# Performance work log

Measured on AMD Instinct MI355X. Metric: run time of the kernel, lower is better.

The kernel has to match this reference:

```python
import jax, jax.numpy as jnp
import numpy as np

B, T, L, H = 512, 512, 64, 512  # batch, time_steps, sequence_len, hidden_dim


def gru_cell(x, h, W_ih, W_hh, b_ih, b_hh):
    # PyTorch GRUCell math. W_ih: [3H, in], W_hh: [3H, H]; gate order (r, z, n).
    gi = x @ W_ih.T + b_ih
    gh = h @ W_hh.T + b_hh
    i_r, i_z, i_n = jnp.split(gi, 3, axis=-1)
    h_r, h_z, h_n = jnp.split(gh, 3, axis=-1)
    r = jax.nn.sigmoid(i_r + h_r)
    z = jax.nn.sigmoid(i_z + h_z)
    n = jnp.tanh(i_n + r * h_n)
    return (1.0 - z) * n + z * h


def setup_inputs() -> dict:
    key = jax.random.key(0)
    ks = jax.random.split(key, 12)
    s = 1.0 / np.sqrt(H)  # PyTorch GRUCell/Linear init scale
    u = lambda k, shape: jax.random.uniform(k, shape, jnp.float32, -s, s)
    return {
        "x": jax.random.normal(ks[0], (B, T + L - 1), jnp.float32),
        "h_1": jnp.zeros((B, H), jnp.float32),
        "h_2": jnp.zeros((B, H), jnp.float32),
        "W_ih1": u(ks[1], (3 * H, T)),
        "W_hh1": u(ks[2], (3 * H, H)),
        "b_ih1": u(ks[3], (3 * H,)),
        "b_hh1": u(ks[4], (3 * H,)),
        "W_ih2": u(ks[5], (3 * H, H)),
        "W_hh2": u(ks[6], (3 * H, H)),
        "b_ih2": u(ks[7], (3 * H,)),
        "b_hh2": u(ks[8], (3 * H,)),
        "W_fc": u(ks[9], (1, H)),
        "b_fc": u(ks[10], (1,)),
    }


def reference(x, h_1, h_2, W_ih1, W_hh1, b_ih1, b_hh1,
              W_ih2, W_hh2, b_ih2, b_hh2, W_fc, b_fc):
    # Sliding windows x[:, t:t+T] for t in [0, L): gather once, scan over steps.
    idx = jnp.arange(L)[:, None] + jnp.arange(T)[None, :]  # [L, T]
    xs = jnp.transpose(x[:, idx], (1, 0, 2))  # [L, B, T]

    def step(carry, x_t):
        h1, h2 = carry
        h1 = gru_cell(x_t, h1, W_ih1, W_hh1, b_ih1, b_hh1)
        h2 = gru_cell(h1, h2, W_ih2, W_hh2, b_ih2, b_hh2)
        y = (h2 @ W_fc.T + b_fc)[:, 0]  # [B]
        return (h1, h2), y

    (h1, h2), ys = jax.lax.scan(step, (h_1, h_2), xs)
    return ys.T, h1, h2  # output_seq [B, L], final hidden states
```

## Files before the change

### kernel.cpp

```cpp
#include <hip/hip_runtime.h>
#include <hip/hip_bf16.h>
#include <math.h>

typedef __attribute__((ext_vector_type(8))) short short8;
typedef __attribute__((ext_vector_type(4))) float f32x4;
typedef unsigned short u16;
typedef unsigned int u32;

__device__ __forceinline__ u16 f2bf(float f) {
  union { float f; u32 u; } x; x.f = f;
  return (u16)((x.u + 0x7fffu + ((x.u >> 16) & 1u)) >> 16);
}
__device__ __forceinline__ float sigm(float v) { return 1.0f / (1.0f + __expf(-v)); }

#define MFMA __builtin_amdgcn_mfma_f32_16x16x32_bf16
#define HS 262144

#define LDG16_BODY(FL)                                        \
    "global_load_dwordx4 %0, %16, off " FL "\n\t"             \
    "global_load_dwordx4 %1, %16, off offset:64 " FL "\n\t"   \
    "global_load_dwordx4 %2, %16, off offset:128 " FL "\n\t"  \
    "global_load_dwordx4 %3, %16, off offset:192 " FL "\n\t"  \
    "global_load_dwordx4 %4, %16, off offset:256 " FL "\n\t"  \
    "global_load_dwordx4 %5, %16, off offset:320 " FL "\n\t"  \
    "global_load_dwordx4 %6, %16, off offset:384 " FL "\n\t"  \
    "global_load_dwordx4 %7, %16, off offset:448 " FL "\n\t"  \
    "global_load_dwordx4 %8, %16, off offset:512 " FL "\n\t"  \
    "global_load_dwordx4 %9, %16, off offset:576 " FL "\n\t"  \
    "global_load_dwordx4 %10, %16, off offset:640 " FL "\n\t" \
    "global_load_dwordx4 %11, %16, off offset:704 " FL "\n\t" \
    "global_load_dwordx4 %12, %16, off offset:768 " FL "\n\t" \
    "global_load_dwordx4 %13, %16, off offset:832 " FL "\n\t" \
    "global_load_dwordx4 %14, %16, off offset:896 " FL "\n\t" \
    "global_load_dwordx4 %15, %16, off offset:960 " FL "\n\t" \
    "s_waitcnt vmcnt(0)"
#define LDG16_OPS(a, base)                                                     \
    : "=&v"(a[0]), "=&v"(a[1]), "=&v"(a[2]), "=&v"(a[3]), "=&v"(a[4]),         \
      "=&v"(a[5]), "=&v"(a[6]), "=&v"(a[7]), "=&v"(a[8]), "=&v"(a[9]),         \
      "=&v"(a[10]), "=&v"(a[11]), "=&v"(a[12]), "=&v"(a[13]), "=&v"(a[14]),    \
      "=&v"(a[15])                                                             \
    : "v"(base) : "memory"

__device__ __forceinline__ void ldg16_sc0(short8 a[16], const u16* base) {
  asm volatile(LDG16_BODY("sc0") LDG16_OPS(a, base));
}
__device__ __forceinline__ void ldg16_sc01(short8 a[16], const u16* base) {
  asm volatile(LDG16_BODY("sc0 sc1") LDG16_OPS(a, base));
}
__device__ __forceinline__ void stg_sc01(u32* p, u32 v) {
  asm volatile("global_store_dword %0, %1, off sc0 sc1" :: "v"(p), "v"(v) : "memory");
}

__device__ __forceinline__ void waits_nf(unsigned* a, unsigned ta, unsigned* b, unsigned tb) {
  if (threadIdx.x == 0) {
    while (__hip_atomic_load(a, __ATOMIC_RELAXED, __HIP_MEMORY_SCOPE_AGENT) < ta)
      __builtin_amdgcn_s_sleep(1);
    while (__hip_atomic_load(b, __ATOMIC_RELAXED, __HIP_MEMORY_SCOPE_AGENT) < tb)
      __builtin_amdgcn_s_sleep(1);
  }
  __syncthreads();
}

__global__ __launch_bounds__(256, 1) void gru_fused(
    const float* __restrict__ xin, const float* __restrict__ h1in, const float* __restrict__ h2in,
    const float* __restrict__ Wih1, const float* __restrict__ Whh1,
    const float* __restrict__ bih1, const float* __restrict__ bhh1,
    const float* __restrict__ Wih2, const float* __restrict__ Whh2,
    const float* __restrict__ bih2, const float* __restrict__ bhh2,
    const float* __restrict__ Wfc, const float* __restrict__ bfc,
    float* __restrict__ out, u16* __restrict__ wsb, unsigned* __restrict__ barc)
{
  const int bid   = blockIdx.x;
  const int rb    = bid & 3;
  const int layer = (bid >> 2) & 1;
  const int cbl   = bid >> 3;
  const int n0    = cbl * 16;
  const int wid   = bid >> 2;
  const int tid   = threadIdx.x;
  const int w     = tid >> 6;
  const int lane  = tid & 63;
  const int quad  = lane >> 4;
  const int m16   = lane & 15;

  u16* x0  = wsb;
  u16* x1  = x0 + 512 * 576;
  u16* h1r = x1 + 512 * 576;
  u16* h2r = h1r + 4 * HS;
  u16* h1m = h2r + 4 * HS;

  __shared__ short8 wlds[96 * 64];

  unsigned* c0    = barc + rb * 32;
  unsigned* c1    = barc + 256 + rb * 32;
  unsigned* cinit = barc + 512;

  const float* Wih = layer ? Wih2 : Wih1;
  const float* Whh = layer ? Whh2 : Whh1;
  const float* bih = layer ? bih2 : bih1;
  const float* bhh = layer ? bhh2 : bhh1;

  for (int i = wid * 256 + tid; i < 128 * 575; i += 64 * 256) {
    int r = i / 575, c = i - r * 575;
    int row = rb * 128 + r;
    u16 bv = f2bf(xin[row * 575 + c]);
    x0[row * 576 + c] = bv;
    if (c >= 1) x1[row * 576 + (c - 1)] = bv;
  }
  for (int i = wid * 256 + tid; i < 128 * 512; i += 64 * 256) {
    int r = i >> 9, c = i & 511;
    int row = rb * 128 + r;
    u16 h1v = f2bf(h1in[row * 512 + c]);
    h1r[3 * HS + row * 512 + c] = h1v;
    h2r[3 * HS + row * 512 + c] = f2bf(h2in[row * 512 + c]);
  }
  for (int i = tid; i < 96 * 64; i += 256) {
    int blk = i >> 6, l = i & 63;
    int s, gr;
    if (blk < 64) { s = blk & 31; gr = (blk >> 5) * 512; }
    else          { s = blk - 64; gr = 1024; }
    int n  = n0 + (l & 15);
    int k0 = s * 32 + (l >> 4) * 8;
    short8 pk;
    #pragma unroll
    for (int j = 0; j < 8; ++j) {
      int k = k0 + j;
      float v = (k < 512) ? Wih[(gr + n) * 512 + k] : Whh[(gr + n) * 512 + (k - 512)];
      pk[j] = (short)f2bf(v);
    }
    wlds[blk * 64 + l] = pk;
  }

  float hreg[2][4];
  const float* hin = layer ? h2in : h1in;
  #pragma unroll
  for (int rf = 0; rf < 2; ++rf)
    #pragma unroll
    for (int q = 0; q < 4; ++q)
      hreg[rf][q] = hin[(rb * 128 + (2 * w + rf) * 16 + quad * 4 + q) * 512 + n0 + m16];

  const int nn = n0 + m16;
  const float bias_r  = bih[nn] + bhh[nn];
  const float bias_z  = bih[512 + nn] + bhh[512 + nn];
  const float bias_in = bih[1024 + nn];
  const float bias_hn = bhh[1024 + nn];
  const float wfc  = Wfc[nn];
  const float bfcv = bfc[0];

  __syncthreads();
  if (tid == 0) {
    __builtin_amdgcn_fence(__ATOMIC_RELEASE, "agent");
    __hip_atomic_fetch_add(cinit, 1u, __ATOMIC_RELAXED, __HIP_MEMORY_SCOPE_AGENT);
    while (__hip_atomic_load(cinit, __ATOMIC_RELAXED, __HIP_MEMORY_SCOPE_AGENT) < 256u)
      __builtin_amdgcn_s_sleep(1);
    __builtin_amdgcn_fence(__ATOMIC_ACQUIRE, "agent");
  }
  __syncthreads();

  const int arow0 = rb * 128 + (2 * w) * 16 + m16;
  const int arow1 = arow0 + 16;

  if (layer == 0) {
    for (int u = 0; u < 64; ++u) {
      f32x4 acc[2][4] = {};
      {
        const int c = u & 1;
        const u16* xc = c ? x1 : x0;
        const u32* pa0 = (const u32*)(xc + (size_t)arow0 * 576 + (u - c) + quad * 8);
        const u32* pa1 = (const u32*)(xc + (size_t)arow1 * 576 + (u - c) + quad * 8);
        #pragma unroll
        for (int s = 0; s < 16; ++s) {
          union { short8 v; u32 u4[4]; } a0, a1;
          #pragma unroll
          for (int j = 0; j < 4; ++j) { a0.u4[j] = pa0[s * 16 + j]; a1.u4[j] = pa1[s * 16 + j]; }
          short8 br = wlds[(s)      * 64 + lane];
          short8 bz = wlds[(32 + s) * 64 + lane];
          short8 bi = wlds[(64 + s) * 64 + lane];
          acc[0][0] = MFMA(a0.v, br, acc[0][0], 0, 0, 0);
          acc[1][0] = MFMA(a1.v, br, acc[1][0], 0, 0, 0);
          acc[0][1] = MFMA(a0.v, bz, acc[0][1], 0, 0, 0);
          acc[1][1] = MFMA(a1.v, bz, acc[1][1], 0, 0, 0);
          acc[0][2] = MFMA(a0.v, bi, acc[0][2], 0, 0, 0);
          acc[1][2] = MFMA(a1.v, bi, acc[1][2], 0, 0, 0);
        }
      }
      waits_nf(c0, 32u * (unsigned)u, c1, u >= 4 ? 32u * (unsigned)(u - 3) : 0u);
      #pragma unroll
      for (int rf = 0; rf < 2; ++rf) {
        short8 a[16];
        const u16* base = h1r + (size_t)((u + 3) & 3) * HS +
                          (size_t)(rf ? arow1 : arow0) * 512 + quad * 8;
        ldg16_sc0(a, base);
        #pragma unroll
        for (int s = 0; s < 16; ++s) {
          short8 br = wlds[(16 + s) * 64 + lane];
          short8 bz = wlds[(48 + s) * 64 + lane];
          short8 bh = wlds[(80 + s) * 64 + lane];
          acc[rf][0] = MFMA(a[s], br, acc[rf][0], 0, 0, 0);
          acc[rf][1] = MFMA(a[s], bz, acc[rf][1], 0, 0, 0);
          acc[rf][3] = MFMA(a[s], bh, acc[rf][3], 0, 0, 0);
        }
      }
      {
        u16* hw = h1r + (size_t)(u & 3) * HS;
        u32* hm = (u32*)(h1m + (size_t)(u & 3) * HS);
        #pragma unroll
        for (int rf = 0; rf < 2; ++rf)
          #pragma unroll
          for (int q = 0; q < 4; ++q) {
            float rg = sigm(acc[rf][0][q] + bias_r);
            float zg = sigm(acc[rf][1][q] + bias_z);
            float ng = tanhf(acc[rf][2][q] + bias_in + rg * (acc[rf][3][q] + bias_hn));
            float hv = (1.0f - zg) * ng + zg * hreg[rf][q];
            hreg[rf][q] = hv;
            int row = rb * 128 + (2 * w + rf) * 16 + quad * 4 + q;
            u16 b = f2bf(hv);
            hw[row * 512 + nn] = b;
            int pb = __shfl_xor((int)(u32)b, 1);
            if (!(m16 & 1))
              stg_sc01(&hm[(row * 512 + nn) >> 1], (u32)b | ((u32)(u16)pb << 16));
          }
      }
      asm volatile("s_waitcnt vmcnt(0)" ::: "memory");
      __syncthreads();
      if (tid == 0)
        __hip_atomic_fetch_add(c0, 1u, __ATOMIC_RELAXED, __HIP_MEMORY_SCOPE_AGENT);
    }
  } else {
    for (int v = 0; v < 64; ++v) {
      f32x4 acc[2][4] = {};
      waits_nf(c1, 32u * (unsigned)v, c0, 32u * (unsigned)(v + 1));
      #pragma unroll
      for (int rf = 0; rf < 2; ++rf) {
        short8 a[16];
        const u16* base = h2r + (size_t)((v + 3) & 3) * HS +
                          (size_t)(rf ? arow1 : arow0) * 512 + quad * 8;
        ldg16_sc0(a, base);
        #pragma unroll
        for (int s = 0; s < 16; ++s) {
          short8 br = wlds[(16 + s) * 64 + lane];
          short8 bz = wlds[(48 + s) * 64 + lane];
          short8 bh = wlds[(80 + s) * 64 + lane];
          acc[rf][0] = MFMA(a[s], br, acc[rf][0], 0, 0, 0);
          acc[rf][1] = MFMA(a[s], bz, acc[rf][1], 0, 0, 0);
          acc[rf][3] = MFMA(a[s], bh, acc[rf][3], 0, 0, 0);
        }
      }
      #pragma unroll
      for (int rf = 0; rf < 2; ++rf) {
        short8 a[16];
        const u16* base = h1m + (size_t)(v & 3) * HS +
                          (size_t)(rf ? arow1 : arow0) * 512 + quad * 8;
        ldg16_sc01(a, base);
        #pragma unroll
        for (int s = 0; s < 16; ++s) {
          short8 br = wlds[(s)      * 64 + lane];
          short8 bz = wlds[(32 + s) * 64 + lane];
          short8 bi = wlds[(64 + s) * 64 + lane];
          acc[rf][0] = MFMA(a[s], br, acc[rf][0], 0, 0, 0);
          acc[rf][1] = MFMA(a[s], bz, acc[rf][1], 0, 0, 0);
          acc[rf][2] = MFMA(a[s], bi, acc[rf][2], 0, 0, 0);
        }
      }
      {
        u16* hw = h2r + (size_t)(v & 3) * HS;
        #pragma unroll
        for (int rf = 0; rf < 2; ++rf)
          #pragma unroll
          for (int q = 0; q < 4; ++q) {
            float rg = sigm(acc[rf][0][q] + bias_r);
            float zg = sigm(acc[rf][1][q] + bias_z);
            float ng = tanhf(acc[rf][2][q] + bias_in + rg * (acc[rf][3][q] + bias_hn));
            float hv = (1.0f - zg) * ng + zg * hreg[rf][q];
            hreg[rf][q] = hv;
            int row = rb * 128 + (2 * w + rf) * 16 + quad * 4 + q;
            hw[row * 512 + nn] = f2bf(hv);
          }
      }
      __syncthreads();
      if (tid == 0)
        __hip_atomic_fetch_add(c1, 1u, __ATOMIC_RELAXED, __HIP_MEMORY_SCOPE_AGENT);
      #pragma unroll
      for (int rf = 0; rf < 2; ++rf)
        #pragma unroll
        for (int q = 0; q < 4; ++q) {
          float yv = hreg[rf][q] * wfc;
          yv += __shfl_xor(yv, 1);
          yv += __shfl_xor(yv, 2);
          yv += __shfl_xor(yv, 4);
          yv += __shfl_xor(yv, 8);
          if (m16 == 0) {
            int row = rb * 128 + (2 * w + rf) * 16 + quad * 4 + q;
            atomicAdd(&out[row * 64 + v], yv + (n0 == 0 ? bfcv : 0.0f));
          }
        }
    }
  }

  float* hout = out + 32768 + layer * (512 * 512);
  #pragma unroll
  for (int rf = 0; rf < 2; ++rf)
    #pragma unroll
    for (int q = 0; q < 4; ++q) {
      int row = rb * 128 + (2 * w + rf) * 16 + quad * 4 + q;
      hout[row * 512 + nn] = hreg[rf][q];
    }
}

extern "C" void kernel_launch(void* const* d_in, const int* in_sizes, int n_in,
                              void* d_out, int out_size, void* d_ws, size_t ws_size,
                              hipStream_t stream) {
  (void)in_sizes; (void)n_in; (void)out_size; (void)ws_size;
  hipMemsetAsync(d_out, 0, 32768 * sizeof(float), stream);
  hipMemsetAsync(d_ws, 0, 4096, stream);
  unsigned* bar = (unsigned*)d_ws;
  u16* wsb = (u16*)((char*)d_ws + 4096);
  gru_fused<<<256, 256, 0, stream>>>(
      (const float*)d_in[0], (const float*)d_in[1], (const float*)d_in[2],
      (const float*)d_in[3], (const float*)d_in[4], (const float*)d_in[5], (const float*)d_in[6],
      (const float*)d_in[7], (const float*)d_in[8], (const float*)d_in[9], (const float*)d_in[10],
      (const float*)d_in[11], (const float*)d_in[12],
      (float*)d_out, wsb, bar);
}
```

Before: 815.7 us.

## Replace atomic counter barriers with per-block flag arrays and split load waits

Replaces the shared atomic-counter barriers with per-column-block flag slots that each block writes with a plain sc0 sc1 store. Waiters poll all 32 flags in parallel with one wave-wide load and a ballot, which removes atomic contention. It also issues both row-fragment loads before waiting and uses a partial vmcnt wait so the first MFMA chain overlaps the second load. Layer 2 now waits on layer 1 only after its own recurrent half, hidden stores are packed into 32-bit writes, and sigmoid/tanh use rcp-based fast approximations. The risks are the memory ordering of plain flag stores without explicit fences, and a small loss of accuracy in the activations.

```diff
diff --git a/kernel.cpp b/kernel.cpp
--- a/kernel.cpp
+++ b/kernel.cpp
@@ -11,7 +11,12 @@
   union { float f; u32 u; } x; x.f = f;
   return (u16)((x.u + 0x7fffu + ((x.u >> 16) & 1u)) >> 16);
 }
-__device__ __forceinline__ float sigm(float v) { return 1.0f / (1.0f + __expf(-v)); }
+__device__ __forceinline__ float sigm(float v) {
+  return __builtin_amdgcn_rcpf(1.0f + __expf(-v));
+}
+__device__ __forceinline__ float tanh_fast(float v) {
+  return 1.0f - 2.0f * __builtin_amdgcn_rcpf(1.0f + __expf(2.0f * v));
+}
 
 #define MFMA __builtin_amdgcn_mfma_f32_16x16x32_bf16
 #define HS 262144
@@ -32,8 +37,7 @@
     "global_load_dwordx4 %12, %16, off offset:768 " FL "\n\t" \
     "global_load_dwordx4 %13, %16, off offset:832 " FL "\n\t" \
     "global_load_dwordx4 %14, %16, off offset:896 " FL "\n\t" \
-    "global_load_dwordx4 %15, %16, off offset:960 " FL "\n\t" \
-    "s_waitcnt vmcnt(0)"
+    "global_load_dwordx4 %15, %16, off offset:960 " FL
 #define LDG16_OPS(a, base)                                                     \
     : "=&v"(a[0]), "=&v"(a[1]), "=&v"(a[2]), "=&v"(a[3]), "=&v"(a[4]),         \
       "=&v"(a[5]), "=&v"(a[6]), "=&v"(a[7]), "=&v"(a[8]), "=&v"(a[9]),         \
@@ -41,24 +45,41 @@
       "=&v"(a[15])                                                             \
     : "v"(base) : "memory"
 
-__device__ __forceinline__ void ldg16_sc0(short8 a[16], const u16* base) {
+__device__ __forceinline__ void ldg16nw_sc0(short8 a[16], const u16* base) {
   asm volatile(LDG16_BODY("sc0") LDG16_OPS(a, base));
 }
-__device__ __forceinline__ void ldg16_sc01(short8 a[16], const u16* base) {
+__device__ __forceinline__ void ldg16nw_sc01(short8 a[16], const u16* base) {
   asm volatile(LDG16_BODY("sc0 sc1") LDG16_OPS(a, base));
 }
+#define VMCNT16() do { asm volatile("s_waitcnt vmcnt(16)" ::: "memory"); \
+                       __builtin_amdgcn_sched_barrier(0); } while (0)
+#define VMCNT0()  do { asm volatile("s_waitcnt vmcnt(0)"  ::: "memory"); \
+                       __builtin_amdgcn_sched_barrier(0); } while (0)
+
 __device__ __forceinline__ void stg_sc01(u32* p, u32 v) {
   asm volatile("global_store_dword %0, %1, off sc0 sc1" :: "v"(p), "v"(v) : "memory");
 }
-
-__device__ __forceinline__ void waits_nf(unsigned* a, unsigned ta, unsigned* b, unsigned tb) {
-  if (threadIdx.x == 0) {
-    while (__hip_atomic_load(a, __ATOMIC_RELAXED, __HIP_MEMORY_SCOPE_AGENT) < ta)
-      __builtin_amdgcn_s_sleep(1);
-    while (__hip_atomic_load(b, __ATOMIC_RELAXED, __HIP_MEMORY_SCOPE_AGENT) < tb)
-      __builtin_amdgcn_s_sleep(1);
-  }
-  __syncthreads();
+__device__ __forceinline__ u32 ldflag(const u32* p) {
+  u32 v;
+  asm volatile("global_load_dword %0, %1, off sc0 sc1\n\t"
+               "s_waitcnt vmcnt(0)" : "=v"(v) : "v"(p) : "memory");
+  return v;
+}
+
+__device__ __forceinline__ u32 wait_ge(const u32* flags, u32 target, int lane) {
+  const u32* p = flags + (lane & 31);
+  u32 v;
+  for (;;) {
+    v = ldflag(p);
+    if (__ballot(v >= target) == ~0ull) break;
+    __builtin_amdgcn_s_sleep(1);
+  }
+  #pragma unroll
+  for (int k = 16; k; k >>= 1) {
+    u32 o = (u32)__shfl_xor((int)v, k);
+    v = v < o ? v : o;
+  }
+  return v;
 }
 
 __global__ __launch_bounds__(256, 1) void gru_fused(
@@ -90,8 +111,8 @@
 
   __shared__ short8 wlds[96 * 64];
 
-  unsigned* c0    = barc + rb * 32;
-  unsigned* c1    = barc + 256 + rb * 32;
+  u32* f0    = (u32*)barc + rb * 32;
+  u32* f1    = (u32*)barc + 128 + rb * 32;
   unsigned* cinit = barc + 512;
 
   const float* Wih = layer ? Wih2 : Wih1;
@@ -160,7 +181,9 @@
   const int arow1 = arow0 + 16;
 
   if (layer == 0) {
+    u32 c1min = 0;
     for (int u = 0; u < 64; ++u) {
+      if (u >= 4 && c1min < (u32)(u - 3)) c1min = wait_ge(f1, (u32)(u - 3), lane);
       f32x4 acc[2][4] = {};
       {
         const int c = u & 1;
@@ -183,102 +206,138 @@
           acc[1][2] = MFMA(a1.v, bi, acc[1][2], 0, 0, 0);
         }
       }
-      waits_nf(c0, 32u * (unsigned)u, c1, u >= 4 ? 32u * (unsigned)(u - 3) : 0u);
-      #pragma unroll
-      for (int rf = 0; rf < 2; ++rf) {
-        short8 a[16];
-        const u16* base = h1r + (size_t)((u + 3) & 3) * HS +
-                          (size_t)(rf ? arow1 : arow0) * 512 + quad * 8;
-        ldg16_sc0(a, base);
+      if (u > 0) wait_ge(f0, (u32)u, lane); else VMCNT0();
+      {
+        short8 a0[16], a1[16];
+        const u16* hb = h1r + (size_t)((u + 3) & 3) * HS + quad * 8;
+        ldg16nw_sc0(a0, hb + (size_t)arow0 * 512);
+        ldg16nw_sc0(a1, hb + (size_t)arow1 * 512);
+        VMCNT16();
         #pragma unroll
         for (int s = 0; s < 16; ++s) {
           short8 br = wlds[(16 + s) * 64 + lane];
           short8 bz = wlds[(48 + s) * 64 + lane];
           short8 bh = wlds[(80 + s) * 64 + lane];
-          acc[rf][0] = MFMA(a[s], br, acc[rf][0], 0, 0, 0);
-          acc[rf][1] = MFMA(a[s], bz, acc[rf][1], 0, 0, 0);
-          acc[rf][3] = MFMA(a[s], bh, acc[rf][3], 0, 0, 0);
-        }
-      }
-      {
-        u16* hw = h1r + (size_t)(u & 3) * HS;
-        u32* hm = (u32*)(h1m + (size_t)(u & 3) * HS);
+          acc[0][0] = MFMA(a0[s], br, acc[0][0], 0, 0, 0);
+          acc[0][1] = MFMA(a0[s], bz, acc[0][1], 0, 0, 0);
+          acc[0][3] = MFMA(a0[s], bh, acc[0][3], 0, 0, 0);
+        }
+        VMCNT0();
+        #pragma unroll
+        for (int s = 0; s < 16; ++s) {
+          short8 br = wlds[(16 + s) * 64 + lane];
+          short8 bz = wlds[(48 + s) * 64 + lane];
+          short8 bh = wlds[(80 + s) * 64 + lane];
+          acc[1][0] = MFMA(a1[s], br, acc[1][0], 0, 0, 0);
+          acc[1][1] = MFMA(a1[s], bz, acc[1][1], 0, 0, 0);
+          acc[1][3] = MFMA(a1[s], bh, acc[1][3], 0, 0, 0);
+        }
+      }
+      {
+        u32* hw32 = (u32*)(h1r + (size_t)(u & 3) * HS);
+        u32* hm   = (u32*)(h1m + (size_t)(u & 3) * HS);
         #pragma unroll
         for (int rf = 0; rf < 2; ++rf)
           #pragma unroll
           for (int q = 0; q < 4; ++q) {
             float rg = sigm(acc[rf][0][q] + bias_r);
             float zg = sigm(acc[rf][1][q] + bias_z);
-            float ng = tanhf(acc[rf][2][q] + bias_in + rg * (acc[rf][3][q] + bias_hn));
+            float ng = tanh_fast(acc[rf][2][q] + bias_in + rg * (acc[rf][3][q] + bias_hn));
             float hv = (1.0f - zg) * ng + zg * hreg[rf][q];
             hreg[rf][q] = hv;
             int row = rb * 128 + (2 * w + rf) * 16 + quad * 4 + q;
             u16 b = f2bf(hv);
-            hw[row * 512 + nn] = b;
             int pb = __shfl_xor((int)(u32)b, 1);
-            if (!(m16 & 1))
-              stg_sc01(&hm[(row * 512 + nn) >> 1], (u32)b | ((u32)(u16)pb << 16));
+            if (!(m16 & 1)) {
+              u32 pr = (u32)b | ((u32)(u16)pb << 16);
+              int pi = (row * 512 + nn) >> 1;
+              hw32[pi] = pr;
+              stg_sc01(&hm[pi], pr);
+            }
           }
       }
       asm volatile("s_waitcnt vmcnt(0)" ::: "memory");
       __syncthreads();
-      if (tid == 0)
-        __hip_atomic_fetch_add(c0, 1u, __ATOMIC_RELAXED, __HIP_MEMORY_SCOPE_AGENT);
+      if (tid == 0) stg_sc01(&f0[cbl], (u32)(u + 1));
     }
   } else {
     for (int v = 0; v < 64; ++v) {
       f32x4 acc[2][4] = {};
-      waits_nf(c1, 32u * (unsigned)v, c0, 32u * (unsigned)(v + 1));
-      #pragma unroll
-      for (int rf = 0; rf < 2; ++rf) {
-        short8 a[16];
-        const u16* base = h2r + (size_t)((v + 3) & 3) * HS +
-                          (size_t)(rf ? arow1 : arow0) * 512 + quad * 8;
-        ldg16_sc0(a, base);
+      if (v > 0) wait_ge(f1, (u32)v, lane); else VMCNT0();
+      {
+        short8 a0[16], a1[16];
+        const u16* hb = h2r + (size_t)((v + 3) & 3) * HS + quad * 8;
+        ldg16nw_sc0(a0, hb + (size_t)arow0 * 512);
+        ldg16nw_sc0(a1, hb + (size_t)arow1 * 512);
+        VMCNT16();
         #pragma unroll
         for (int s = 0; s < 16; ++s) {
           short8 br = wlds[(16 + s) * 64 + lane];
           short8 bz = wlds[(48 + s) * 64 + lane];
           short8 bh = wlds[(80 + s) * 64 + lane];
-          acc[rf][0] = MFMA(a[s], br, acc[rf][0], 0, 0, 0);
-          acc[rf][1] = MFMA(a[s], bz, acc[rf][1], 0, 0, 0);
-          acc[rf][3] = MFMA(a[s], bh, acc[rf][3], 0, 0, 0);
-        }
-      }
-      #pragma unroll
-      for (int rf = 0; rf < 2; ++rf) {
-        short8 a[16];
-        const u16* base = h1m + (size_t)(v & 3) * HS +
-                          (size_t)(rf ? arow1 : arow0) * 512 + quad * 8;
-        ldg16_sc01(a, base);
+          acc[0][0] = MFMA(a0[s], br, acc[0][0], 0, 0, 0);
+          acc[0][1] = MFMA(a0[s], bz, acc[0][1], 0, 0, 0);
+          acc[0][3] = MFMA(a0[s], bh, acc[0][3], 0, 0, 0);
+        }
+        VMCNT0();
+        #pragma unroll
+        for (int s = 0; s < 16; ++s) {
+          short8 br = wlds[(16 + s) * 64 + lane];
+          short8 bz = wlds[(48 + s) * 64 + lane];
+          short8 bh = wlds[(80 + s) * 64 + lane];
+          acc[1][0] = MFMA(a1[s], br, acc[1][0], 0, 0, 0);
+          acc[1][1] = MFMA(a1[s], bz, acc[1][1], 0, 0, 0);
+          acc[1][3] = MFMA(a1[s], bh, acc[1][3], 0, 0, 0);
+        }
+      }
+      wait_ge(f0, (u32)(v + 1), lane);
+      {
+        short8 a0[16], a1[16];
+        const u16* hb = h1m + (size_t)(v & 3) * HS + quad * 8;
+        ldg16nw_sc01(a0, hb + (size_t)arow0 * 512);
+        ldg16nw_sc01(a1, hb + (size_t)arow1 * 512);
+        VMCNT16();
         #pragma unroll
         for (int s = 0; s < 16; ++s) {
           short8 br = wlds[(s)      * 64 + lane];
           short8 bz = wlds[(32 + s) * 64 + lane];
           short8 bi = wlds[(64 + s) * 64 + lane];
-          acc[rf][0] = MFMA(a[s], br, acc[rf][0], 0, 0, 0);
-          acc[rf][1] = MFMA(a[s], bz, acc[rf][1], 0, 0, 0);
-          acc[rf][2] = MFMA(a[s], bi, acc[rf][2], 0, 0, 0);
-        }
-      }
-      {
-        u16* hw = h2r + (size_t)(v & 3) * HS;
+          acc[0][0] = MFMA(a0[s], br, acc[0][0], 0, 0, 0);
+          acc[0][1] = MFMA(a0[s], bz, acc[0][1], 0, 0, 0);
+          acc[0][2] = MFMA(a0[s], bi, acc[0][2], 0, 0, 0);
+        }
+        VMCNT0();
+        #pragma unroll
+        for (int s = 0; s < 16; ++s) {
+          short8 br = wlds[(s)      * 64 + lane];
+          short8 bz = wlds[(32 + s) * 64 + lane];
+          short8 bi = wlds[(64 + s) * 64 + lane];
+          acc[1][0] = MFMA(a1[s], br, acc[1][0], 0, 0, 0);
+          acc[1][1] = MFMA(a1[s], bz, acc[1][1], 0, 0, 0);
+          acc[1][2] = MFMA(a1[s], bi, acc[1][2], 0, 0, 0);
+        }
+      }
+      {
+        u32* hw32 = (u32*)(h2r + (size_t)(v & 3) * HS);
         #pragma unroll
         for (int rf = 0; rf < 2; ++rf)
           #pragma unroll
           for (int q = 0; q < 4; ++q) {
             float rg = sigm(acc[rf][0][q] + bias_r);
             float zg = sigm(acc[rf][1][q] + bias_z);
-            float ng = tanhf(acc[rf][2][q] + bias_in + rg * (acc[rf][3][q] + bias_hn));
+            float ng = tanh_fast(acc[rf][2][q] + bias_in + rg * (acc[rf][3][q] + bias_hn));
             float hv = (1.0f - zg) * ng + zg * hreg[rf][q];
             hreg[rf][q] = hv;
             int row = rb * 128 + (2 * w + rf) * 16 + quad * 4 + q;
-            hw[row * 512 + nn] = f2bf(hv);
+            u16 b = f2bf(hv);
+            int pb = __shfl_xor((int)(u32)b, 1);
+            if (!(m16 & 1))
+              hw32[(row * 512 + nn) >> 1] = (u32)b | ((u32)(u16)pb << 16);
           }
       }
+      asm volatile("s_waitcnt vmcnt(0)" ::: "memory");
       __syncthreads();
-      if (tid == 0)
-        __hip_atomic_fetch_add(c1, 1u, __ATOMIC_RELAXED, __HIP_MEMORY_SCOPE_AGENT);
+      if (tid == 0) stg_sc01(&f1[cbl], (u32)(v + 1));
       #pragma unroll
       for (int rf = 0; rf < 2; ++rf)
         #pragma unroll
```

Measured after the change: 828.5 us. About the same (+1.6%).

## Fuse both GRU layers per workgroup with row-group split and global weight streaming

Applied to the files above, without the earlier changes.

Instead of dedicating workgroups to layer 1 or layer 2, each workgroup now computes both layers for a 64-row batch slice and 16 hidden columns. Half the bf16 weights stay in LDS and the other half are pre-packed to global memory and streamed with nontemporal loads. Hidden-state ring buffers shrink to double buffers. The output projection is done by one column group as a dot product over the full h2 row, replacing atomicAdd. It also adds faster rcp-based sigmoid/tanh and splits the load waits so MFMAs overlap outstanding loads. The aim is better use of each CU and less inter-layer barrier latency, at the cost of extra global weight traffic every step.

```diff
diff --git a/kernel.cpp b/kernel.cpp
--- a/kernel.cpp
+++ b/kernel.cpp
@@ -11,10 +11,16 @@
   union { float f; u32 u; } x; x.f = f;
   return (u16)((x.u + 0x7fffu + ((x.u >> 16) & 1u)) >> 16);
 }
-__device__ __forceinline__ float sigm(float v) { return 1.0f / (1.0f + __expf(-v)); }
+__device__ __forceinline__ float sigm(float v) {
+  return __builtin_amdgcn_rcpf(1.0f + __expf(-v));
+}
+__device__ __forceinline__ float tanh_fast(float v) {
+  return 1.0f - 2.0f * __builtin_amdgcn_rcpf(1.0f + __expf(2.0f * v));
+}
 
 #define MFMA __builtin_amdgcn_mfma_f32_16x16x32_bf16
-#define HS 262144
+#define XS  (512*576)
+#define HSL (512*512)
 
 #define LDG16_BODY(FL)                                        \
     "global_load_dwordx4 %0, %16, off " FL "\n\t"             \
@@ -32,8 +38,7 @@
     "global_load_dwordx4 %12, %16, off offset:768 " FL "\n\t" \
     "global_load_dwordx4 %13, %16, off offset:832 " FL "\n\t" \
     "global_load_dwordx4 %14, %16, off offset:896 " FL "\n\t" \
-    "global_load_dwordx4 %15, %16, off offset:960 " FL "\n\t" \
-    "s_waitcnt vmcnt(0)"
+    "global_load_dwordx4 %15, %16, off offset:960 " FL
 #define LDG16_OPS(a, base)                                                     \
     : "=&v"(a[0]), "=&v"(a[1]), "=&v"(a[2]), "=&v"(a[3]), "=&v"(a[4]),         \
       "=&v"(a[5]), "=&v"(a[6]), "=&v"(a[7]), "=&v"(a[8]), "=&v"(a[9]),         \
@@ -41,15 +46,12 @@
       "=&v"(a[15])                                                             \
     : "v"(base) : "memory"
 
-__device__ __forceinline__ void ldg16_sc0(short8 a[16], const u16* base) {
+__device__ __forceinline__ void ldg16nw_sc0(short8 a[16], const u16* base) {
   asm volatile(LDG16_BODY("sc0") LDG16_OPS(a, base));
 }
-__device__ __forceinline__ void ldg16_sc01(short8 a[16], const u16* base) {
-  asm volatile(LDG16_BODY("sc0 sc1") LDG16_OPS(a, base));
-}
-__device__ __forceinline__ void stg_sc01(u32* p, u32 v) {
-  asm volatile("global_store_dword %0, %1, off sc0 sc1" :: "v"(p), "v"(v) : "memory");
-}
+
+#define VMCNT(N) do { asm volatile("s_waitcnt vmcnt(" #N ")" ::: "memory"); \
+                      __builtin_amdgcn_sched_barrier(0); } while (0)
 
 __device__ __forceinline__ void waits_nf(unsigned* a, unsigned ta, unsigned* b, unsigned tb) {
   if (threadIdx.x == 0) {
@@ -60,6 +62,34 @@
   }
   __syncthreads();
 }
+
+__device__ __forceinline__ float ydot(const short8 a[16], const float* wfcl, int quad) {
+  float y = 0.0f;
+  #pragma unroll
+  for (int s = 0; s < 16; ++s) {
+    const float4 wa = *(const float4*)&wfcl[32 * s + quad * 8];
+    const float4 wb = *(const float4*)&wfcl[32 * s + quad * 8 + 4];
+    union { short8 v; u32 u4[4]; } aa; aa.v = a[s];
+    #pragma unroll
+    for (int k = 0; k < 4; ++k) {
+      union { u32 u; float f; } lo, hi;
+      lo.u = aa.u4[k] << 16;
+      hi.u = aa.u4[k] & 0xffff0000u;
+      float w0 = (k < 2) ? ((k & 1) ? wa.z : wa.x) : ((k & 1) ? wb.z : wb.x);
+      float w1 = (k < 2) ? ((k & 1) ? wa.w : wa.y) : ((k & 1) ? wb.w : wb.y);
+      y = fmaf(lo.f, w0, y);
+      y = fmaf(hi.f, w1, y);
+    }
+  }
+  return y;
+}
+
+#define MFMA3X16_LDS(A, B0, A0, A1, A2) do {                          \
+    _Pragma("unroll")                                                 \
+    for (int s_ = 0; s_ < 16; ++s_) {                                 \
+      A0 = MFMA((A)[s_], wlds[((B0)+s_)*64+lane],    A0, 0, 0, 0);    \
+      A1 = MFMA((A)[s_], wlds[((B0)+16+s_)*64+lane], A1, 0, 0, 0);    \
+      A2 = MFMA((A)[s_], wlds[((B0)+32+s_)*64+lane], A2, 0, 0, 0); } } while (0)
 
 __global__ __launch_bounds__(256, 1) void gru_fused(
     const float* __restrict__ xin, const float* __restrict__ h1in, const float* __restrict__ h2in,
@@ -70,80 +100,89 @@
     const float* __restrict__ Wfc, const float* __restrict__ bfc,
     float* __restrict__ out, u16* __restrict__ wsb, unsigned* __restrict__ barc)
 {
-  const int bid   = blockIdx.x;
-  const int rb    = bid & 3;
-  const int layer = (bid >> 2) & 1;
-  const int cbl   = bid >> 3;
-  const int n0    = cbl * 16;
-  const int wid   = bid >> 2;
-  const int tid   = threadIdx.x;
-  const int w     = tid >> 6;
-  const int lane  = tid & 63;
-  const int quad  = lane >> 4;
-  const int m16   = lane & 15;
+  const int bid  = blockIdx.x;
+  const int g    = bid & 7;
+  const int wgi  = bid >> 3;
+  const int n0   = wgi * 16;
+  const int tid  = threadIdx.x;
+  const int w    = tid >> 6;
+  const int lane = tid & 63;
+  const int quad = lane >> 4;
+  const int m16  = lane & 15;
+  const int R0   = g * 64;
+  const int xrow = R0 + w * 16 + m16;
+  const int nn   = n0 + m16;
 
   u16* x0  = wsb;
-  u16* x1  = x0 + 512 * 576;
-  u16* h1r = x1 + 512 * 576;
-  u16* h2r = h1r + 4 * HS;
-  u16* h1m = h2r + 4 * HS;
+  u16* x1  = x0 + XS;
+  u16* h1r = x1 + XS;
+  u16* h2r = h1r + 2 * HSL;
+  short8* wfx  = (short8*)(h2r + 2 * HSL);
+  short8* wfm1 = wfx + (size_t)wgi * 96 * 64;
+  short8* wfm2 = wfm1 + 48 * 64;
 
   __shared__ short8 wlds[96 * 64];
-
-  unsigned* c0    = barc + rb * 32;
-  unsigned* c1    = barc + 256 + rb * 32;
+  __shared__ float wfcl[512];
+
+  unsigned* cA = barc + g * 32;
+  unsigned* cB = barc + 256 + g * 32;
   unsigned* cinit = barc + 512;
 
-  const float* Wih = layer ? Wih2 : Wih1;
-  const float* Whh = layer ? Whh2 : Whh1;
-  const float* bih = layer ? bih2 : bih1;
-  const float* bhh = layer ? bhh2 : bhh1;
-
-  for (int i = wid * 256 + tid; i < 128 * 575; i += 64 * 256) {
+  for (int i = wgi * 256 + tid; i < 64 * 575; i += 32 * 256) {
     int r = i / 575, c = i - r * 575;
-    int row = rb * 128 + r;
+    int row = R0 + r;
     u16 bv = f2bf(xin[row * 575 + c]);
     x0[row * 576 + c] = bv;
     if (c >= 1) x1[row * 576 + (c - 1)] = bv;
   }
-  for (int i = wid * 256 + tid; i < 128 * 512; i += 64 * 256) {
-    int r = i >> 9, c = i & 511;
-    int row = rb * 128 + r;
-    u16 h1v = f2bf(h1in[row * 512 + c]);
-    h1r[3 * HS + row * 512 + c] = h1v;
-    h2r[3 * HS + row * 512 + c] = f2bf(h2in[row * 512 + c]);
+  for (int i = tid; i < 64 * 16; i += 256) {
+    int r = i >> 4, cL = i & 15;
+    int row = R0 + r, col = n0 + cL;
+    h1r[HSL + row * 512 + col] = f2bf(h1in[row * 512 + col]);
+    h2r[HSL + row * 512 + col] = f2bf(h2in[row * 512 + col]);
   }
   for (int i = tid; i < 96 * 64; i += 256) {
     int blk = i >> 6, l = i & 63;
-    int s, gr;
-    if (blk < 64) { s = blk & 31; gr = (blk >> 5) * 512; }
-    else          { s = blk - 64; gr = 1024; }
-    int n  = n0 + (l & 15);
+    int b = (blk < 48) ? blk : blk - 48;
+    const float* M = blk < 48 ? Wih1 : Whh2;
+    int t = b >> 4, s = b & 15;
+    int gr = t * 512 + n0 + (l & 15);
     int k0 = s * 32 + (l >> 4) * 8;
     short8 pk;
     #pragma unroll
-    for (int j = 0; j < 8; ++j) {
-      int k = k0 + j;
-      float v = (k < 512) ? Wih[(gr + n) * 512 + k] : Whh[(gr + n) * 512 + (k - 512)];
-      pk[j] = (short)f2bf(v);
-    }
+    for (int j = 0; j < 8; ++j) pk[j] = (short)f2bf(M[gr * 512 + k0 + j]);
+    wfm1[blk * 64 + l] = pk;
+  }
+  for (int i = tid; i < 96 * 64; i += 256) {
+    int blk = i >> 6, l = i & 63;
+    int b = (blk < 48) ? blk : blk - 48;
+    const float* M = blk < 48 ? Whh1 : Wih2;
+    int t = b >> 4, s = b & 15;
+    int gr = t * 512 + n0 + (l & 15);
+    int k0 = s * 32 + (l >> 4) * 8;
+    short8 pk;
+    #pragma unroll
+    for (int j = 0; j < 8; ++j) pk[j] = (short)f2bf(M[gr * 512 + k0 + j]);
     wlds[blk * 64 + l] = pk;
   }
-
-  float hreg[2][4];
-  const float* hin = layer ? h2in : h1in;
+  for (int i = tid; i < 512; i += 256) wfcl[i] = Wfc[i];
+
+  float hreg1[4], hreg2[4];
   #pragma unroll
-  for (int rf = 0; rf < 2; ++rf)
-    #pragma unroll
-    for (int q = 0; q < 4; ++q)
-      hreg[rf][q] = hin[(rb * 128 + (2 * w + rf) * 16 + quad * 4 + q) * 512 + n0 + m16];
-
-  const int nn = n0 + m16;
-  const float bias_r  = bih[nn] + bhh[nn];
-  const float bias_z  = bih[512 + nn] + bhh[512 + nn];
-  const float bias_in = bih[1024 + nn];
-  const float bias_hn = bhh[1024 + nn];
-  const float wfc  = Wfc[nn];
+  for (int q = 0; q < 4; ++q) {
+    int row = R0 + w * 16 + quad * 4 + q;
+    hreg1[q] = h1in[row * 512 + nn];
+    hreg2[q] = h2in[row * 512 + nn];
+  }
+
+  const float b1r = bih1[nn] + bhh1[nn];
+  const float b1z = bih1[512 + nn] + bhh1[512 + nn];
+  const float b1i = bih1[1024 + nn];
+  const float b1h = bhh1[1024 + nn];
+  const float b2r = bih2[nn] + bhh2[nn];
+  const float b2z = bih2[512 + nn] + bhh2[512 + nn];
+  const float b2i = bih2[1024 + nn];
+  const float b2h = bhh2[1024 + nn];
   const float bfcv = bfc[0];
 
   __syncthreads();
@@ -156,154 +195,137 @@
   }
   __syncthreads();
 
-  const int arow0 = rb * 128 + (2 * w) * 16 + m16;
-  const int arow1 = arow0 + 16;
-
-  if (layer == 0) {
-    for (int u = 0; u < 64; ++u) {
-      f32x4 acc[2][4] = {};
-      {
-        const int c = u & 1;
-        const u16* xc = c ? x1 : x0;
-        const u32* pa0 = (const u32*)(xc + (size_t)arow0 * 576 + (u - c) + quad * 8);
-        const u32* pa1 = (const u32*)(xc + (size_t)arow1 * 576 + (u - c) + quad * 8);
-        #pragma unroll
-        for (int s = 0; s < 16; ++s) {
-          union { short8 v; u32 u4[4]; } a0, a1;
+  for (int u = 0; u < 64; ++u) {
+    short8 ah[16];
+    ldg16nw_sc0(ah, h1r + (size_t)((u + 1) & 1) * HSL + (size_t)xrow * 512 + quad * 8);
+    f32x4 a1r = {}, a1z = {}, a1i = {}, a1h = {};
+    {
+      const int c = u & 1;
+      const u16* xc = c ? x1 : x0;
+      const u32* pa = (const u32*)(xc + (size_t)xrow * 576 + (u - c) + quad * 8);
+      #pragma unroll
+      for (int hh = 0; hh < 2; ++hh) {
+        u32 av[32];
+        #pragma unroll
+        for (int s = 0; s < 8; ++s)
           #pragma unroll
-          for (int j = 0; j < 4; ++j) { a0.u4[j] = pa0[s * 16 + j]; a1.u4[j] = pa1[s * 16 + j]; }
-          short8 br = wlds[(s)      * 64 + lane];
-          short8 bz = wlds[(32 + s) * 64 + lane];
-          short8 bi = wlds[(64 + s) * 64 + lane];
-          acc[0][0] = MFMA(a0.v, br, acc[0][0], 0, 0, 0);
-          acc[1][0] = MFMA(a1.v, br, acc[1][0], 0, 0, 0);
-          acc[0][1] = MFMA(a0.v, bz, acc[0][1], 0, 0, 0);
-          acc[1][1] = MFMA(a1.v, bz, acc[1][1], 0, 0, 0);
-          acc[0][2] = MFMA(a0.v, bi, acc[0][2], 0, 0, 0);
-          acc[1][2] = MFMA(a1.v, bi, acc[1][2], 0, 0, 0);
+          for (int j = 0; j < 4; ++j) av[s * 4 + j] = pa[(hh * 8 + s) * 16 + j];
+        short8 bx[24];
+        #pragma unroll
+        for (int s = 0; s < 8; ++s) {
+          int ss = hh * 8 + s;
+          bx[s]      = __builtin_nontemporal_load(&wfm1[(ss)      * 64 + lane]);
+          bx[8 + s]  = __builtin_nontemporal_load(&wfm1[(16 + ss) * 64 + lane]);
+          bx[16 + s] = __builtin_nontemporal_load(&wfm1[(32 + ss) * 64 + lane]);
+        }
+        #pragma unroll
+        for (int s = 0; s < 8; ++s) {
+          union { short8 v; u32 u4[4]; } a;
+          #pragma unroll
+          for (int j = 0; j < 4; ++j) a.u4[j] = av[s * 4 + j];
+          a1r = MFMA(a.v, bx[s],      a1r, 0, 0, 0);
+          a1z = MFMA(a.v, bx[8 + s],  a1z, 0, 0, 0);
+          a1i = MFMA(a.v, bx[16 + s], a1i, 0, 0, 0);
         }
       }
-      waits_nf(c0, 32u * (unsigned)u, c1, u >= 4 ? 32u * (unsigned)(u - 3) : 0u);
+    }
+    VMCNT(0);
+    MFMA3X16_LDS(ah, 0, a1r, a1z, a1h);
+    {
+      u32* hw = (u32*)(h1r + (size_t)(u & 1) * HSL);
       #pragma unroll
-      for (int rf = 0; rf < 2; ++rf) {
-        short8 a[16];
-        const u16* base = h1r + (size_t)((u + 3) & 3) * HS +
-                          (size_t)(rf ? arow1 : arow0) * 512 + quad * 8;
-        ldg16_sc0(a, base);
-        #pragma unroll
-        for (int s = 0; s < 16; ++s) {
-          short8 br = wlds[(16 + s) * 64 + lane];
-          short8 bz = wlds[(48 + s) * 64 + lane];
-          short8 bh = wlds[(80 + s) * 64 + lane];
-          acc[rf][0] = MFMA(a[s], br, acc[rf][0], 0, 0, 0);
-          acc[rf][1] = MFMA(a[s], bz, acc[rf][1], 0, 0, 0);
-          acc[rf][3] = MFMA(a[s], bh, acc[rf][3], 0, 0, 0);
+      for (int q = 0; q < 4; ++q) {
+        float rg = sigm(a1r[q] + b1r);
+        float zg = sigm(a1z[q] + b1z);
+        float ng = tanh_fast(a1i[q] + b1i + rg * (a1h[q] + b1h));
+        float hv = (1.0f - zg) * ng + zg * hreg1[q];
+        hreg1[q] = hv;
+        int row = R0 + w * 16 + quad * 4 + q;
+        u16 b = f2bf(hv);
+        int pb = __shfl_xor((int)(u32)b, 1);
+        if (!(m16 & 1))
+          hw[(row * 512 + nn) >> 1] = (u32)b | ((u32)(u16)pb << 16);
+      }
+    }
+    asm volatile("s_waitcnt vmcnt(0)" ::: "memory");
+    __syncthreads();
+    if (tid == 0)
+      __hip_atomic_fetch_add(cA, 1u, __ATOMIC_RELAXED, __HIP_MEMORY_SCOPE_AGENT);
+
+    waits_nf(cA, 32u * (unsigned)(u + 1), cB, 32u * (unsigned)u);
+    short8 bb1[16], bb2[16];
+    ldg16nw_sc0(bb1, h1r + (size_t)(u & 1) * HSL + (size_t)xrow * 512 + quad * 8);
+    ldg16nw_sc0(bb2, h2r + (size_t)((u + 1) & 1) * HSL + (size_t)xrow * 512 + quad * 8);
+    f32x4 a2r = {}, a2z = {}, a2i = {}, a2h = {};
+    VMCNT(16);
+    MFMA3X16_LDS(bb1, 48, a2r, a2z, a2i);
+    VMCNT(0);
+    {
+      #pragma unroll
+      for (int hh = 0; hh < 2; ++hh) {
+        short8 bx[24];
+        #pragma unroll
+        for (int s = 0; s < 8; ++s) {
+          int ss = hh * 8 + s;
+          bx[s]      = __builtin_nontemporal_load(&wfm2[(ss)      * 64 + lane]);
+          bx[8 + s]  = __builtin_nontemporal_load(&wfm2[(16 + ss) * 64 + lane]);
+          bx[16 + s] = __builtin_nontemporal_load(&wfm2[(32 + ss) * 64 + lane]);
+        }
+        #pragma unroll
+        for (int s = 0; s < 8; ++s) {
+          a2r = MFMA(bb2[hh * 8 + s], bx[s],      a2r, 0, 0, 0);
+          a2z = MFMA(bb2[hh * 8 + s], bx[8 + s],  a2z, 0, 0, 0);
+          a2h = MFMA(bb2[hh * 8 + s], bx[16 + s], a2h, 0, 0, 0);
         }
       }
-      {
-        u16* hw = h1r + (size_t)(u & 3) * HS;
-        u32* hm = (u32*)(h1m + (size_t)(u & 3) * HS);
-        #pragma unroll
-        for (int rf = 0; rf < 2; ++rf)
-          #pragma unroll
-          for (int q = 0; q < 4; ++q) {
-            float rg = sigm(acc[rf][0][q] + bias_r);
-            float zg = sigm(acc[rf][1][q] + bias_z);
-            float ng = tanhf(acc[rf][2][q] + bias_in + rg * (acc[rf][3][q] + bias_hn));
-            float hv = (1.0f - zg) * ng + zg * hreg[rf][q];
-            hreg[rf][q] = hv;
-            int row = rb * 128 + (2 * w + rf) * 16 + quad * 4 + q;
-            u16 b = f2bf(hv);
-            hw[row * 512 + nn] = b;
-            int pb = __shfl_xor((int)(u32)b, 1);
-            if (!(m16 & 1))
-              stg_sc01(&hm[(row * 512 + nn) >> 1], (u32)b | ((u32)(u16)pb << 16));
-          }
+    }
+    float ya = 0.0f;
+    if (wgi == 0 && u > 0) ya = ydot(bb2, wfcl, quad);
+    {
+      u32* hw = (u32*)(h2r + (size_t)(u & 1) * HSL);
+      #pragma unroll
+      for (int q = 0; q < 4; ++q) {
+        float rg = sigm(a2r[q] + b2r);
+        float zg = sigm(a2z[q] + b2z);
+        float ng = tanh_fast(a2i[q] + b2i + rg * (a2h[q] + b2h));
+        float hv = (1.0f - zg) * ng + zg * hreg2[q];
+        hreg2[q] = hv;
+        int row = R0 + w * 16 + quad * 4 + q;
+        u16 b = f2bf(hv);
+        int pb = __shfl_xor((int)(u32)b, 1);
+        if (!(m16 & 1))
+          hw[(row * 512 + nn) >> 1] = (u32)b | ((u32)(u16)pb << 16);
       }
-      asm volatile("s_waitcnt vmcnt(0)" ::: "memory");
-      __syncthreads();
-      if (tid == 0)
-        __hip_atomic_fetch_add(c0, 1u, __ATOMIC_RELAXED, __HIP_MEMORY_SCOPE_AGENT);
-    }
-  } else {
-    for (int v = 0; v < 64; ++v) {
-      f32x4 acc[2][4] = {};
-      waits_nf(c1, 32u * (unsigned)v, c0, 32u * (unsigned)(v + 1));
-      #pragma unroll
-      for (int rf = 0; rf < 2; ++rf) {
-        short8 a[16];
-        const u16* base = h2r + (size_t)((v + 3) & 3) * HS +
-                          (size_t)(rf ? arow1 : arow0) * 512 + quad * 8;
-        ldg16_sc0(a, base);
-        #pragma unroll
-        for (int s = 0; s < 16; ++s) {
-          short8 br = wlds[(16 + s) * 64 + lane];
-          short8 bz = wlds[(48 + s) * 64 + lane];
-          short8 bh = wlds[(80 + s) * 64 + lane];
-          acc[rf][0] = MFMA(a[s], br, acc[rf][0], 0, 0, 0);
-          acc[rf][1] = MFMA(a[s], bz, acc[rf][1], 0, 0, 0);
-          acc[rf][3] = MFMA(a[s], bh, acc[rf][3], 0, 0, 0);
-        }
-      }
-      #pragma unroll
-      for (int rf = 0; rf < 2; ++rf) {
-        short8 a[16];
-        const u16* base = h1m + (size_t)(v & 3) * HS +
-                          (size_t)(rf ? arow1 : arow0) * 512 + quad * 8;
-        ldg16_sc01(a, base);
-        #pragma unroll
-        for (int s = 0; s < 16; ++s) {
-          short8 br = wlds[(s)      * 64 + lane];
-          short8 bz = wlds[(32 + s) * 64 + lane];
-          short8 bi = wlds[(64 + s) * 64 + lane];
-          acc[rf][0] = MFMA(a[s], br, acc[rf][0], 0, 0, 0);
-          acc[rf][1] = MFMA(a[s], bz, acc[rf][1], 0, 0, 0);
-          acc[rf][2] = MFMA(a[s], bi, acc[rf][2], 0, 0, 0);
-        }
-      }
-      {
-        u16* hw = h2r + (size_t)(v & 3) * HS;
-        #pragma unroll
-        for (int rf = 0; rf < 2; ++rf)
-          #pragma unroll
-          for (int q = 0; q < 4; ++q) {
-            float rg = sigm(acc[rf][0][q] + bias_r);
-            float zg = sigm(acc[rf][1][q] + bias_z);
-            float ng = tanhf(acc[rf][2][q] + bias_in + rg * (acc[rf][3][q] + bias_hn));
-            float hv = (1.0f - zg) * ng + zg * hreg[rf][q];
-            hreg[rf][q] = hv;
-            int row = rb * 128 + (2 * w + rf) * 16 + quad * 4 + q;
-            hw[row * 512 + nn] = f2bf(hv);
-          }
-      }
-      __syncthreads();
-      if (tid == 0)
-        __hip_atomic_fetch_add(c1, 1u, __ATOMIC_RELAXED, __HIP_MEMORY_SCOPE_AGENT);
-      #pragma unroll
-      for (int rf = 0; rf < 2; ++rf)
-        #pragma unroll
-        for (int q = 0; q < 4; ++q) {
-          float yv = hreg[rf][q] * wfc;
-          yv += __shfl_xor(yv, 1);
-          yv += __shfl_xor(yv, 2);
-          yv += __shfl_xor(yv, 4);
-          yv += __shfl_xor(yv, 8);
-          if (m16 == 0) {
-            int row = rb * 128 + (2 * w + rf) * 16 + quad * 4 + q;
-            atomicAdd(&out[row * 64 + v], yv + (n0 == 0 ? bfcv : 0.0f));
-          }
-        }
-    }
-  }
-
-  float* hout = out + 32768 + layer * (512 * 512);
+    }
+    asm volatile("s_waitcnt vmcnt(0)" ::: "memory");
+    __syncthreads();
+    if (tid == 0)
+      __hip_atomic_fetch_add(cB, 1u, __ATOMIC_RELAXED, __HIP_MEMORY_SCOPE_AGENT);
+    if (wgi == 0 && u > 0) {
+      ya += __shfl_xor(ya, 16);
+      ya += __shfl_xor(ya, 32);
+      if (quad == 0) out[xrow * 64 + (u - 1)] = ya + bfcv;
+    }
+  }
+
+  float* ho1 = out + 32768;
+  float* ho2 = out + 32768 + 262144;
   #pragma unroll
-  for (int rf = 0; rf < 2; ++rf)
-    #pragma unroll
-    for (int q = 0; q < 4; ++q) {
-      int row = rb * 128 + (2 * w + rf) * 16 + quad * 4 + q;
-      hout[row * 512 + nn] = hreg[rf][q];
-    }
+  for (int q = 0; q < 4; ++q) {
+    int row = R0 + w * 16 + quad * 4 + q;
+    ho1[row * 512 + nn] = hreg1[q];
+    ho2[row * 512 + nn] = hreg2[q];
+  }
+  if (wgi == 0) {
+    waits_nf(cB, 32u * 64u, cB, 32u * 64u);
+    short8 bz[16];
+    ldg16nw_sc0(bz, h2r + (size_t)1 * HSL + (size_t)xrow * 512 + quad * 8);
+    VMCNT(0);
+    float ya = ydot(bz, wfcl, quad);
+    ya += __shfl_xor(ya, 16);
+    ya += __shfl_xor(ya, 32);
+    if (quad == 0) out[xrow * 64 + 63] = ya + bfcv;
+  }
 }
 
 extern "C" void kernel_launch(void* const* d_in, const int* in_sizes, int n_in,
```

Result: slower. 1.762 ms (+116.0%).
